# Kernel tuning notes

Measured on AMD Instinct MI355X. Metric: run time of the kernel, lower is better.

## Reference

```python
import jax, jax.numpy as jnp
import numpy as np

B, L, DM = 4, 1024, 1024
ED, N, K, R = 2048, 16, 4, 64  # d_inner, d_state, d_conv, dt_rank


def setup_inputs() -> dict:
    key = jax.random.key(0)
    ks = jax.random.split(key, 9)
    s = lambda i, shape, scale: jax.random.normal(ks[i], shape, jnp.float32) * scale
    inp = s(0, (B, L, DM), 1.0)
    W_in = s(1, (2 * ED, DM), DM ** -0.5)
    conv_w = s(2, (ED, 1, K), 0.5)
    conv_b = s(3, (ED,), 0.1)
    W_x = s(4, (R + 2 * N, ED), ED ** -0.5)
    W_dt = s(5, (ED, R), R ** -0.5)
    # dt bias init as in torch: inverse-softplus of dt ~ LogUniform(1e-3, 1e-1)
    dt = jnp.exp(jax.random.uniform(ks[6], (ED,)) * (np.log(0.1) - np.log(1e-3)) + np.log(1e-3))
    b_dt = dt + jnp.log(-jnp.expm1(-dt))
    A_log = jnp.log(jnp.tile(jnp.arange(1, N + 1, dtype=jnp.float32), (ED, 1)))
    D_param = jnp.ones((ED,), jnp.float32)
    W_out = s(7, (DM, ED), ED ** -0.5)
    return dict(input=inp, W_in=W_in, conv_w=conv_w, conv_b=conv_b, W_x=W_x,
                W_dt=W_dt, b_dt=b_dt, A_log=A_log, D_param=D_param, W_out=W_out)


def reference(input, W_in, conv_w, conv_b, W_x, W_dt, b_dt, A_log, D_param, W_out):
    b = input.shape[0]
    # in_proj -> x, z each [B, L, ED]
    xz = input @ W_in.T
    x, z = jnp.split(xz, 2, axis=-1)
    # causal depthwise conv over time (torch pads K-1 then crops to L == left-pad K-1)
    xc = jnp.transpose(x, (0, 2, 1))  # [B, ED, L]
    xc = jax.lax.conv_general_dilated(
        xc, conv_w, window_strides=(1,), padding=[(K - 1, 0)],
        dimension_numbers=('NCH', 'OIH', 'NCH'), feature_group_count=ED)
    xc = xc + conv_b[None, :, None]
    x = jax.nn.silu(jnp.transpose(xc, (0, 2, 1)))  # [B, L, ED]
    # x_proj -> delta_low, B, C
    dBC = x @ W_x.T  # [B, L, R+2N]
    dlow, Bm, Cm = dBC[..., :R], dBC[..., R:R + N], dBC[..., R + N:]
    # dt_proj (bias folded into softplus, matching delta_bias + delta_softplus)
    delta = jax.nn.softplus(dlow @ W_dt.T + b_dt)  # [B, L, ED]
    A = -jnp.exp(A_log)  # [ED, N]

    def step(h, ins):
        x_t, d_t, B_t, C_t = ins  # [B,ED],[B,ED],[B,N],[B,N]
        dA = jnp.exp(d_t[..., None] * A)           # [B, ED, N]
        h = dA * h + (d_t * x_t)[..., None] * B_t[:, None, :]
        y_t = jnp.einsum('ben,bn->be', h, C_t)
        return h, y_t

    h0 = jnp.zeros((b, ED, N), x.dtype)
    xs = (jnp.moveaxis(x, 1, 0), jnp.moveaxis(delta, 1, 0),
          jnp.moveaxis(Bm, 1, 0), jnp.moveaxis(Cm, 1, 0))
    _, ys = jax.lax.scan(step, h0, xs)
    y = jnp.moveaxis(ys, 0, 1) + D_param * x  # skip connection D*x
    y = y * jax.nn.silu(z)                    # output gating
    return y @ W_out.T                        # out_proj [B, L, DM]
```

## Files before the change

kernel.cpp:

```cpp
#include <hip/hip_runtime.h>
#include <hip/hip_bf16.h>
#include <math.h>

constexpr int Bb = 4, Ls = 1024, DMm = 1024, ED = 2048, Nst = 16, Rr = 64;
constexpr int Mrows = Bb * Ls;
constexpr int XZW = 2 * ED;
constexpr int NC = 32, CL = Ls / NC;

typedef __attribute__((ext_vector_type(8))) short bf16x8;
typedef __attribute__((ext_vector_type(4))) float f32x4;

#define GLOAD_LDS16(gp, lp) __builtin_amdgcn_global_load_lds( \
    (const __attribute__((address_space(1))) void*)(gp), \
    (__attribute__((address_space(3))) void*)(lp), 16, 0, 0)

#define SBAR() do { __builtin_amdgcn_sched_barrier(0); \
                    __builtin_amdgcn_s_barrier(); \
                    __builtin_amdgcn_sched_barrier(0); } while (0)
#define VMCNT4() do { asm volatile("s_waitcnt vmcnt(4)" ::: "memory"); \
                      __builtin_amdgcn_sched_barrier(0); } while (0)
#define VMCNT0() do { asm volatile("s_waitcnt vmcnt(0)" ::: "memory"); \
                      __builtin_amdgcn_sched_barrier(0); } while (0)

static __device__ __forceinline__ unsigned short f2bf(float x) {
    __hip_bfloat16 h = __float2bfloat16(x);
    return *reinterpret_cast<unsigned short*>(&h);
}
static __device__ __forceinline__ float bf2f(unsigned short u) {
    return __uint_as_float(((unsigned)u) << 16);
}

__global__ __launch_bounds__(256)
void cast5(const float* __restrict__ a, unsigned short* __restrict__ oa,
           const float* __restrict__ b, unsigned short* __restrict__ ob,
           const float* __restrict__ c, unsigned short* __restrict__ oc,
           const float* __restrict__ d, unsigned short* __restrict__ odh,
           unsigned short* __restrict__ odl,
           const float* __restrict__ e, unsigned short* __restrict__ oe)
{
    const int bid = blockIdx.x;
    if (bid < 10240) {
        const float* src; unsigned short* dst; int i;
        if (bid < 4096)      { src = a; dst = oa; i = (bid * 256 + threadIdx.x) * 4; }
        else if (bid < 8192) { src = b; dst = ob; i = ((bid - 4096) * 256 + threadIdx.x) * 4; }
        else                 { src = c; dst = oc; i = ((bid - 8192) * 256 + threadIdx.x) * 4; }
        float4 v = *(const float4*)(src + i);
        ushort4 o;
        o.x = f2bf(v.x); o.y = f2bf(v.y); o.z = f2bf(v.z); o.w = f2bf(v.w);
        *(ushort4*)(dst + i) = o;
    } else if (bid < 10368) {
        const int i = ((bid - 10240) * 256 + threadIdx.x) * 4;
        float4 v = *(const float4*)(d + i);
        ushort4 h, lo;
        h.x = f2bf(v.x); h.y = f2bf(v.y); h.z = f2bf(v.z); h.w = f2bf(v.w);
        lo.x = f2bf(v.x - bf2f(h.x)); lo.y = f2bf(v.y - bf2f(h.y));
        lo.z = f2bf(v.z - bf2f(h.z)); lo.w = f2bf(v.w - bf2f(h.w));
        *(ushort4*)(odh + i) = h;
        *(ushort4*)(odl + i) = lo;
    } else {
        const int i = ((bid - 10368) * 256 + threadIdx.x) * 4;
        float4 v = *(const float4*)(e + i);
        ushort4 o;
        o.x = f2bf(v.x); o.y = f2bf(v.y); o.z = f2bf(v.z); o.w = f2bf(v.w);
        *(ushort4*)(oe + i) = o;
    }
}

__global__ __launch_bounds__(512, 2)
void gemm256(const unsigned short* __restrict__ A,
             const unsigned short* __restrict__ B,
             unsigned short* __restrict__ C, int K, int ldc, int nbx)
{
    __shared__ unsigned short lds[65536];

    const int tid = threadIdx.x;
    const int l = tid & 63;
    const int w = tid >> 6;
    const int wm = w >> 2, wn = w & 3;

    const int cpx = gridDim.x >> 3;
    const int wg = (blockIdx.x & 7) * cpx + (blockIdx.x >> 3);
    const int bx = wg % nbx, by = wg / nbx;
    const int row0 = by * 256, col0 = bx * 256;

    const int NT = K >> 6;

    const int sr = l >> 3;
    const int sc = ((l & 7) ^ sr) * 8;
    const unsigned short* gA = A + (size_t)(row0 + sr) * K + sc;
    const unsigned short* gB = B + (size_t)(col0 + sr) * K + sc;

#define STAGE_A(t, h) do { const int b_ = (t) & 1;                              \
    GLOAD_LDS16(gA + (size_t)((h) * 128 + w * 16) * K + (t) * 64,              \
                &lds[b_ * 32768 + ((h) * 128 + w * 16) * 64 + l * 8]);          \
    GLOAD_LDS16(gA + (size_t)((h) * 128 + w * 16 + 8) * K + (t) * 64,          \
                &lds[b_ * 32768 + ((h) * 128 + w * 16 + 8) * 64 + l * 8]);      \
} while (0)
#define STAGE_B(t, h) do { const int b_ = (t) & 1;                              \
    GLOAD_LDS16(gB + (size_t)((h) * 128 + w * 16) * K + (t) * 64,              \
                &lds[b_ * 32768 + 16384 + ((h) * 128 + w * 16) * 64 + l * 8]);  \
    GLOAD_LDS16(gB + (size_t)((h) * 128 + w * 16 + 8) * K + (t) * 64,          \
                &lds[b_ * 32768 + 16384 + ((h) * 128 + w * 16 + 8) * 64 + l * 8]); \
} while (0)

    const int r15 = l & 15, kl = l >> 4, l7 = l & 7;

    f32x4 acc[8][4] = {};

    STAGE_A(0, 0); STAGE_B(0, 0); STAGE_A(0, 1); STAGE_B(0, 1);
    if (NT > 1) { STAGE_A(1, 0); STAGE_B(1, 0); VMCNT4(); }
    else        { VMCNT0(); }
    SBAR();

    for (int t = 0; t < NT; ++t) {
        const int base = (t & 1) * 32768;
        #pragma unroll
        for (int p = 0; p < 4; ++p) {
            const int mq = p >> 1, nq = p & 1;

            bf16x8 af[4][2], bfr[2][2];
            #pragma unroll
            for (int mf = 0; mf < 4; ++mf)
                #pragma unroll
                for (int ks = 0; ks < 2; ++ks) {
                    const int row = mq * 128 + wm * 64 + mf * 16 + r15;
                    const int slot = (ks * 4 + kl) ^ l7;
                    af[mf][ks] = *(const bf16x8*)&lds[base + row * 64 + slot * 8];
                }
            #pragma unroll
            for (int nf = 0; nf < 2; ++nf)
                #pragma unroll
                for (int ks = 0; ks < 2; ++ks) {
                    const int row = nq * 128 + wn * 32 + nf * 16 + r15;
                    const int slot = (ks * 4 + kl) ^ l7;
                    bfr[nf][ks] = *(const bf16x8*)&lds[base + 16384 + row * 64 + slot * 8];
                }

            if (p == 0 && t + 1 < NT) STAGE_A(t + 1, 1);
            if (p == 1 && t + 1 < NT) STAGE_B(t + 1, 1);
            if (p == 2 && t + 2 < NT) STAGE_A(t + 2, 0);
            if (p == 3 && t + 2 < NT) STAGE_B(t + 2, 0);

            __builtin_amdgcn_s_setprio(1);
            #pragma unroll
            for (int mf = 0; mf < 4; ++mf)
                #pragma unroll
                for (int nf = 0; nf < 2; ++nf)
                    #pragma unroll
                    for (int ks = 0; ks < 2; ++ks)
                        acc[mq * 4 + mf][nq * 2 + nf] =
                            __builtin_amdgcn_mfma_f32_16x16x32_bf16(
                                af[mf][ks], bfr[nf][ks],
                                acc[mq * 4 + mf][nq * 2 + nf], 0, 0, 0);
            __builtin_amdgcn_s_setprio(0);

            if (p < 3) {
                SBAR();
            } else {
                if (t + 2 < NT)      { VMCNT4(); SBAR(); }
                else if (t + 1 < NT) { VMCNT0(); SBAR(); }
            }
        }
    }

    const int crow = (l >> 4) * 4;
    #pragma unroll
    for (int am = 0; am < 8; ++am) {
        const int mq = am >> 2, mf = am & 3;
        #pragma unroll
        for (int bn = 0; bn < 4; ++bn) {
            const int nq = bn >> 1, nf = bn & 1;
            const int r = row0 + mq * 128 + wm * 64 + mf * 16 + crow;
            const int c = col0 + nq * 128 + wn * 32 + nf * 16 + r15;
            #pragma unroll
            for (int q = 0; q < 4; ++q)
                C[(size_t)(r + q) * ldc + c] = f2bf(acc[am][bn][q]);
        }
    }
#undef STAGE_A
#undef STAGE_B
}

__global__ __launch_bounds__(256)
void gemm_out(const unsigned short* __restrict__ A,
              const unsigned short* __restrict__ B,
              float* __restrict__ C, int K, int ldc)
{
    __shared__ unsigned short lds[2][(128 + 64) * 64];

    const int tid = threadIdx.x;
    const int l = tid & 63, w = tid >> 6;
    const int wm = w >> 1, wn = w & 1;
    const int row0 = blockIdx.y * 128, col0 = blockIdx.x * 64;

    const int sr = l >> 3;
    const int scS = ((l & 7) ^ sr) * 8;
    const unsigned short* gA = A + (size_t)(row0 + sr) * K + scS;
    const unsigned short* gB = B + (size_t)(col0 + sr) * K + scS;

#define STAGE6(t, bsel) do {                                                   \
    const size_t kt_ = (size_t)(t) * 64;                                       \
    _Pragma("unroll")                                                          \
    for (int i_ = 0; i_ < 4; ++i_) {                                           \
        const int rA_ = w * 32 + i_ * 8;                                       \
        GLOAD_LDS16(gA + (size_t)rA_ * K + kt_, &lds[(bsel)][rA_ * 64 + l * 8]); } \
    _Pragma("unroll")                                                          \
    for (int i_ = 0; i_ < 2; ++i_) {                                           \
        const int rB_ = w * 16 + i_ * 8;                                       \
        GLOAD_LDS16(gB + (size_t)rB_ * K + kt_, &lds[(bsel)][8192 + rB_ * 64 + l * 8]); } \
} while (0)

    const int r15 = l & 15, kl = l >> 4;
    const int NT = K >> 6;

    f32x4 acc[4][2] = {};

    STAGE6(0, 0);
    __syncthreads();

    int buf = 0;
    for (int t = 0; t < NT; ++t) {
        if (t + 1 < NT) STAGE6(t + 1, buf ^ 1);

        bf16x8 a[4][2], b[2][2];
        #pragma unroll
        for (int mf = 0; mf < 4; ++mf)
            #pragma unroll
            for (int ks = 0; ks < 2; ++ks) {
                const int row = wm * 64 + mf * 16 + r15;
                const int slot = (ks * 4 + kl) ^ (row & 7);
                a[mf][ks] = *(const bf16x8*)&lds[buf][row * 64 + slot * 8];
            }
        #pragma unroll
        for (int nf = 0; nf < 2; ++nf)
            #pragma unroll
            for (int ks = 0; ks < 2; ++ks) {
                const int row = wn * 32 + nf * 16 + r15;
                const int slot = (ks * 4 + kl) ^ (row & 7);
                b[nf][ks] = *(const bf16x8*)&lds[buf][8192 + row * 64 + slot * 8];
            }

        #pragma unroll
        for (int mf = 0; mf < 4; ++mf)
            #pragma unroll
            for (int nf = 0; nf < 2; ++nf)
                #pragma unroll
                for (int ks = 0; ks < 2; ++ks)
                    acc[mf][nf] = __builtin_amdgcn_mfma_f32_16x16x32_bf16(
                        a[mf][ks], b[nf][ks], acc[mf][nf], 0, 0, 0);

        __syncthreads();
        buf ^= 1;
    }

    const int crow = (l >> 4) * 4;
    #pragma unroll
    for (int mf = 0; mf < 4; ++mf)
        #pragma unroll
        for (int nf = 0; nf < 2; ++nf) {
            const int r = row0 + wm * 64 + mf * 16 + crow;
            const int c = col0 + wn * 32 + nf * 16 + r15;
            #pragma unroll
            for (int q = 0; q < 4; ++q)
                C[(size_t)(r + q) * ldc + c] = acc[mf][nf][q];
        }
#undef STAGE6
}

__global__ __launch_bounds__(256)
void gemm_bc(const unsigned short* __restrict__ A,
             const unsigned short* __restrict__ B,
             float* __restrict__ part)
{
    __shared__ unsigned short sA[2][128 * 64];
    __shared__ unsigned short sB[2][96 * 64];

    const int tid = threadIdx.x;
    const int l = tid & 63, w = tid >> 6;
    const int wm = w >> 1, wn = w & 1;
    const int row0 = blockIdx.y * 128;
    const int k0 = blockIdx.z * 256;

    const int lr = l >> 3;
    const int scS = ((l & 7) ^ lr) * 8;
    const int ldsOff = lr * 64 + (l & 7) * 8;

#define STAGE_BC(t, bsel) do {                                                  \
    const int kb_ = k0 + (t) * 64;                                              \
    _Pragma("unroll")                                                           \
    for (int p_ = 0; p_ < 4; ++p_) {                                            \
        const int r_ = p_ * 32 + w * 8;                                         \
        GLOAD_LDS16(A + (size_t)(row0 + r_ + lr) * 2048 + kb_ + scS,           \
                    &sA[(bsel)][r_ * 64 + ldsOff]); }                           \
    _Pragma("unroll")                                                           \
    for (int p_ = 0; p_ < 3; ++p_) {                                            \
        const int r_ = p_ * 32 + w * 8;                                         \
        GLOAD_LDS16(B + (size_t)(r_ + lr) * 2048 + kb_ + scS,                  \
                    &sB[(bsel)][r_ * 64 + ldsOff]); }                           \
} while (0)

    const int r15 = l & 15, kl = l >> 4;
    f32x4 acc[4][3] = {};

    STAGE_BC(0, 0);
    __syncthreads();

    int buf = 0;
    #pragma unroll
    for (int t = 0; t < 4; ++t) {
        if (t + 1 < 4) STAGE_BC(t + 1, buf ^ 1);

        bf16x8 a[4][2], b[3][2];
        #pragma unroll
        for (int mf = 0; mf < 4; ++mf)
            #pragma unroll
            for (int ks = 0; ks < 2; ++ks) {
                const int row = wm * 64 + mf * 16 + r15;
                const int slot = (ks * 4 + kl) ^ (row & 7);
                a[mf][ks] = *(const bf16x8*)&sA[buf][row * 64 + slot * 8];
            }
        #pragma unroll
        for (int nf = 0; nf < 3; ++nf)
            #pragma unroll
            for (int ks = 0; ks < 2; ++ks) {
                const int row = wn * 48 + nf * 16 + r15;
                const int slot = (ks * 4 + kl) ^ (row & 7);
                b[nf][ks] = *(const bf16x8*)&sB[buf][row * 64 + slot * 8];
            }

        #pragma unroll
        for (int mf = 0; mf < 4; ++mf)
            #pragma unroll
            for (int nf = 0; nf < 3; ++nf)
                #pragma unroll
                for (int ks = 0; ks < 2; ++ks)
                    acc[mf][nf] = __builtin_amdgcn_mfma_f32_16x16x32_bf16(
                        a[mf][ks], b[nf][ks], acc[mf][nf], 0, 0, 0);

        __syncthreads();
        buf ^= 1;
    }

    float* Cp = part + (size_t)blockIdx.z * (Mrows * 96);
    const int crow = (l >> 4) * 4;
    #pragma unroll
    for (int mf = 0; mf < 4; ++mf)
        #pragma unroll
        for (int nf = 0; nf < 3; ++nf) {
            const int r = row0 + wm * 64 + mf * 16 + crow;
            const int c = wn * 48 + nf * 16 + r15;
            #pragma unroll
            for (int q = 0; q < 4; ++q)
                Cp[(size_t)(r + q) * 96 + c] = acc[mf][nf][q];
        }
#undef STAGE_BC
}

__global__ __launch_bounds__(256)
void gemm_dt(const unsigned short* __restrict__ Ah,
             const unsigned short* __restrict__ Al,
             const unsigned short* __restrict__ Bh,
             const unsigned short* __restrict__ Bl,
             const float* __restrict__ bias,
             float* __restrict__ C)
{
    __shared__ unsigned short sAh[128 * 64], sAl[128 * 64];
    __shared__ unsigned short sBh[128 * 64], sBl[128 * 64];

    const int tid = threadIdx.x;
    const int l = tid & 63, w = tid >> 6;
    const int wm = w >> 1, wn = w & 1;
    const int row0 = blockIdx.y * 128, col0 = blockIdx.x * 128;

    const int lr = l >> 3;
    const int scS = ((l & 7) ^ lr) * 8;
    const int ldsOff = lr * 64 + (l & 7) * 8;

    #pragma unroll
    for (int p = 0; p < 4; ++p) {
        const int r = p * 32 + w * 8;
        GLOAD_LDS16(Ah + (size_t)(row0 + r + lr) * 64 + scS, &sAh[r * 64 + ldsOff]);
        GLOAD_LDS16(Al + (size_t)(row0 + r + lr) * 64 + scS, &sAl[r * 64 + ldsOff]);
        GLOAD_LDS16(Bh + (size_t)(col0 + r + lr) * 64 + scS, &sBh[r * 64 + ldsOff]);
        GLOAD_LDS16(Bl + (size_t)(col0 + r + lr) * 64 + scS, &sBl[r * 64 + ldsOff]);
    }
    __syncthreads();

    const int r15 = l & 15, kl = l >> 4;

    bf16x8 ah[4][2], al[4][2];
    #pragma unroll
    for (int mf = 0; mf < 4; ++mf)
        #pragma unroll
        for (int ks = 0; ks < 2; ++ks) {
            const int row = wm * 64 + mf * 16 + r15;
            const int slot = (ks * 4 + kl) ^ (row & 7);
            ah[mf][ks] = *(const bf16x8*)&sAh[row * 64 + slot * 8];
            al[mf][ks] = *(const bf16x8*)&sAl[row * 64 + slot * 8];
        }

    f32x4 acc[4][4] = {};
    #pragma unroll
    for (int nf = 0; nf < 4; ++nf) {
        bf16x8 bh[2], blo[2];
        #pragma unroll
        for (int ks = 0; ks < 2; ++ks) {
            const int row = wn * 64 + nf * 16 + r15;
            const int slot = (ks * 4 + kl) ^ (row & 7);
            bh[ks]  = *(const bf16x8*)&sBh[row * 64 + slot * 8];
            blo[ks] = *(const bf16x8*)&sBl[row * 64 + slot * 8];
        }
        #pragma unroll
        for (int mf = 0; mf < 4; ++mf)
            #pragma unroll
            for (int ks = 0; ks < 2; ++ks) {
                acc[mf][nf] = __builtin_amdgcn_mfma_f32_16x16x32_bf16(
                    ah[mf][ks], bh[ks], acc[mf][nf], 0, 0, 0);
                acc[mf][nf] = __builtin_amdgcn_mfma_f32_16x16x32_bf16(
                    ah[mf][ks], blo[ks], acc[mf][nf], 0, 0, 0);
                acc[mf][nf] = __builtin_amdgcn_mfma_f32_16x16x32_bf16(
                    al[mf][ks], bh[ks], acc[mf][nf], 0, 0, 0);
            }
    }

    const int crow = (l >> 4) * 4;
    #pragma unroll
    for (int mf = 0; mf < 4; ++mf)
        #pragma unroll
        for (int nf = 0; nf < 4; ++nf) {
            const int r = row0 + wm * 64 + mf * 16 + crow;
            const int c = col0 + wn * 64 + nf * 16 + r15;
            const float bb = bias[c];
            #pragma unroll
            for (int q = 0; q < 4; ++q) {
                float v = acc[mf][nf][q] + bb;
                v = (v > 20.f) ? v : log1pf(__expf(v));
                C[(size_t)(r + q) * 2048 + c] = v;
            }
        }
}

__global__ __launch_bounds__(256)
void reduce8(const float* __restrict__ part, float* __restrict__ outp,
             unsigned short* __restrict__ dlh, unsigned short* __restrict__ dll)
{
    constexpr size_t stride = (size_t)Mrows * 96;
    const size_t i = ((size_t)blockIdx.x * 256 + threadIdx.x) * 4;
    float4 s = *(const float4*)(part + i);
    #pragma unroll
    for (int k = 1; k < 8; ++k) {
        float4 v = *(const float4*)(part + k * stride + i);
        s.x += v.x; s.y += v.y; s.z += v.z; s.w += v.w;
    }
    *(float4*)(outp + i) = s;

    const int col = (int)(i % 96);
    if (col < 64) {
        const size_t row = i / 96;
        ushort4 h, lo;
        h.x = f2bf(s.x); h.y = f2bf(s.y); h.z = f2bf(s.z); h.w = f2bf(s.w);
        lo.x = f2bf(s.x - bf2f(h.x)); lo.y = f2bf(s.y - bf2f(h.y));
        lo.z = f2bf(s.z - bf2f(h.z)); lo.w = f2bf(s.w - bf2f(h.w));
        const size_t o = row * 64 + col;
        *(ushort4*)(dlh + o) = h;
        *(ushort4*)(dll + o) = lo;
    }
}

__global__ __launch_bounds__(256)
void conv_silu(const unsigned short* __restrict__ xz, const float* __restrict__ w,
               const float* __restrict__ cbias, unsigned short* __restrict__ out)
{
    const int idx = blockIdx.x * 256 + threadIdx.x;
    const int e = idx & (ED - 1);
    const int rq = idx >> 11;
    const int b = rq >> 8;
    const int l0 = (rq & 255) * 4;

    const unsigned short* base = xz + ((size_t)(b * Ls + l0)) * XZW + e;
    const float w0 = w[e * 4 + 0], w1 = w[e * 4 + 1],
                w2 = w[e * 4 + 2], w3 = w[e * 4 + 3];
    const float cb = cbias[e];

    float xm3 = 0.f, xm2 = 0.f, xm1 = 0.f;
    if (l0 > 0) {
        xm3 = bf2f(base[(ptrdiff_t)(-3) * XZW]);
        xm2 = bf2f(base[(ptrdiff_t)(-2) * XZW]);
        xm1 = bf2f(base[(ptrdiff_t)(-1) * XZW]);
    }
    const float x0 = bf2f(base[0]);
    const float x1 = bf2f(base[(size_t)1 * XZW]);
    const float x2 = bf2f(base[(size_t)2 * XZW]);
    const float x3 = bf2f(base[(size_t)3 * XZW]);

    float y[4];
    y[0] = cb + w0 * xm3 + w1 * xm2 + w2 * xm1 + w3 * x0;
    y[1] = cb + w0 * xm2 + w1 * xm1 + w2 * x0  + w3 * x1;
    y[2] = cb + w0 * xm1 + w1 * x0  + w2 * x1  + w3 * x2;
    y[3] = cb + w0 * x0  + w1 * x1  + w2 * x2  + w3 * x3;

    unsigned short* op = out + ((size_t)(b * Ls + l0)) * ED + e;
    #pragma unroll
    for (int j = 0; j < 4; ++j)
        op[(size_t)j * ED] = f2bf(y[j] / (1.f + __expf(-y[j])));
}

__global__ __launch_bounds__(256)
void scan_phaseA(const unsigned short* __restrict__ xconv,
                 const float* __restrict__ delta,
                 const float* __restrict__ dBC,
                 const float* __restrict__ A_log,
                 float* __restrict__ hA,
                 float* __restrict__ PA)
{
    __shared__ float sB[CL][16];
    const int t = threadIdx.x;
    const int e = blockIdx.x * 256 + t;
    const int ck = blockIdx.y;
    const int b = blockIdx.z;
    const int row0 = b * Ls + ck * CL;

    if (t < CL * 4) {
        const int r = t >> 2, c4 = (t & 3) * 4;
        *(float4*)&sB[r][c4] =
            *(const float4*)&dBC[(size_t)(row0 + r) * 96 + Rr + c4];
    }
    __syncthreads();

    float Ae[16];
    #pragma unroll
    for (int n = 0; n < 16; ++n) Ae[n] = -__expf(A_log[e * 16 + n]);

    float h[16] = {};
    float S = 0.f;
    const float* dp = delta + (size_t)row0 * ED + e;
    const unsigned short* xp = xconv + (size_t)row0 * ED + e;

    #pragma unroll 4
    for (int l = 0; l < CL; ++l) {
        const float d  = dp[(size_t)l * ED];
        const float xv = bf2f(xp[(size_t)l * ED]);
        const float dx = d * xv;
        S += d;
        const float4* bl = (const float4*)&sB[l][0];
        float Bv[16];
        #pragma unroll
        for (int q = 0; q < 4; ++q) {
            float4 t4 = bl[q];
            Bv[4*q] = t4.x; Bv[4*q+1] = t4.y; Bv[4*q+2] = t4.z; Bv[4*q+3] = t4.w;
        }
        #pragma unroll
        for (int n = 0; n < 16; ++n) {
            const float dA = __expf(d * Ae[n]);
            h[n] = fmaf(dA, h[n], dx * Bv[n]);
        }
    }

    float* hp = hA + ((size_t)(b * NC + ck) * 16) * ED + e;
    float* pp = PA + ((size_t)(b * NC + ck) * 16) * ED + e;
    #pragma unroll
    for (int n = 0; n < 16; ++n) {
        hp[(size_t)n * ED] = h[n];
        pp[(size_t)n * ED] = __expf(S * Ae[n]);
    }
}

__global__ __launch_bounds__(256)
void scan_phaseB(float* __restrict__ hA, const float* __restrict__ PA)
{
    const int id = blockIdx.x * 256 + threadIdx.x;
    const int e = id & (ED - 1);
    const int n = (id >> 11) & 15;
    const int b = id >> 15;
    float h = 0.f;
    #pragma unroll
    for (int c = 0; c < NC; ++c) {
        const size_t o = ((size_t)((b * NC + c) * 16 + n)) * ED + e;
        const float loc = hA[o];
        hA[o] = h;
        h = fmaf(PA[o], h, loc);
    }
}

__global__ __launch_bounds__(256)
void scan_phaseC(const unsigned short* __restrict__ xconv,
                 const float* __restrict__ delta,
                 const float* __restrict__ dBC,
                 const unsigned short* __restrict__ xz,
                 const float* __restrict__ A_log,
                 const float* __restrict__ Dp,
                 const float* __restrict__ hA,
                 unsigned short* __restrict__ ybf)
{
    __shared__ float sBC[CL][32];
    const int t = threadIdx.x;
    const int e = blockIdx.x * 256 + t;
    const int ck = blockIdx.y;
    const int b = blockIdx.z;
    const int row0 = b * Ls + ck * CL;

    {
        const int r = t >> 3, c4 = (t & 7) * 4;
        *(float4*)&sBC[r][c4] =
            *(const float4*)&dBC[(size_t)(row0 + r) * 96 + Rr + c4];
    }
    __syncthreads();

    float Ae[16];
    #pragma unroll
    for (int n = 0; n < 16; ++n) Ae[n] = -__expf(A_log[e * 16 + n]);
    const float De = Dp[e];

    float h[16];
    const float* hp = hA + ((size_t)(b * NC + ck) * 16) * ED + e;
    #pragma unroll
    for (int n = 0; n < 16; ++n) h[n] = hp[(size_t)n * ED];

    const float* dp = delta + (size_t)row0 * ED + e;
    const unsigned short* xp = xconv + (size_t)row0 * ED + e;
    const unsigned short* zp = xz + (size_t)row0 * XZW + ED + e;
    unsigned short* yp = ybf + (size_t)row0 * ED + e;

    #pragma unroll 2
    for (int l = 0; l < CL; ++l) {
        const float d  = dp[(size_t)l * ED];
        const float xv = bf2f(xp[(size_t)l * ED]);
        const float dx = d * xv;
        const float4* bl = (const float4*)&sBC[l][0];
        float Bv[16], Cv[16];
        #pragma unroll
        for (int q = 0; q < 4; ++q) {
            float4 t4 = bl[q];
            Bv[4*q] = t4.x; Bv[4*q+1] = t4.y; Bv[4*q+2] = t4.z; Bv[4*q+3] = t4.w;
            float4 u4 = bl[4 + q];
            Cv[4*q] = u4.x; Cv[4*q+1] = u4.y; Cv[4*q+2] = u4.z; Cv[4*q+3] = u4.w;
        }
        float yv = 0.f;
        #pragma unroll
        for (int n = 0; n < 16; ++n) {
            const float dA = __expf(d * Ae[n]);
            h[n] = fmaf(dA, h[n], dx * Bv[n]);
            yv = fmaf(h[n], Cv[n], yv);
        }
        const float zv = bf2f(zp[(size_t)l * XZW]);
        const float sz = zv / (1.f + __expf(-zv));
        yp[(size_t)l * ED] = f2bf((yv + De * xv) * sz);
    }
}

extern "C" void kernel_launch(void* const* d_in, const int* in_sizes, int n_in,
                              void* d_out, int out_size, void* d_ws, size_t ws_size,
                              hipStream_t stream)
{
    const float* input  = (const float*)d_in[0];
    const float* W_in   = (const float*)d_in[1];
    const float* conv_w = (const float*)d_in[2];
    const float* conv_b = (const float*)d_in[3];
    const float* W_x    = (const float*)d_in[4];
    const float* W_dt   = (const float*)d_in[5];
    const float* b_dt   = (const float*)d_in[6];
    const float* A_log  = (const float*)d_in[7];
    const float* Dp     = (const float*)d_in[8];
    const float* W_out  = (const float*)d_in[9];
    float* out = (float*)d_out;
    float* ws  = (float*)d_ws;

    float* xzR   = ws;
    float* xconv = xzR   + (size_t)16777216;
    float* dBC   = xconv + (size_t)8388608;
    float* delta = dBC   + (size_t)393216;
    float* hA    = delta + (size_t)8388608;
    float* PA    = hA    + (size_t)4194304;
    float* wob   = PA    + (size_t)4194304;
    float* extra = wob   + (size_t)1048576;

    unsigned short* xz_bf   = (unsigned short*)xzR;
    unsigned short* xconv_bf= (unsigned short*)xconv;
    unsigned short* in_bf   = (unsigned short*)(xconv + 4194304);
    unsigned short* Win_bf  = (unsigned short*)(xconv + 6291456);
    unsigned short* Wout_bf = (unsigned short*)wob;
    float*          parts   = hA;
    unsigned short* y_bf    = (unsigned short*)PA;

    unsigned short* dlow_hi = (unsigned short*)extra;
    unsigned short* dlow_lo = dlow_hi + 262144;
    unsigned short* Wdt_hi  = dlow_lo + 262144;
    unsigned short* Wdt_lo  = Wdt_hi + 131072;
    unsigned short* Wx_bf   = Wdt_lo + 131072;

    const dim3 blk(256);

    cast5<<<10560, blk, 0, stream>>>(input, in_bf, W_in, Win_bf, W_out, Wout_bf,
                                     W_dt, Wdt_hi, Wdt_lo, W_x, Wx_bf);

    gemm256<<<(XZW / 256) * (Mrows / 256), dim3(512), 0, stream>>>(
        in_bf, Win_bf, xz_bf, DMm, XZW, XZW / 256);

    conv_silu<<<(Mrows / 4) * ED / 256, blk, 0, stream>>>(
        xz_bf, conv_w, conv_b, xconv_bf);

    gemm_bc<<<dim3(1, Mrows / 128, 8), blk, 0, stream>>>(xconv_bf, Wx_bf, parts);
    reduce8<<<(Mrows * 96) / 1024, blk, 0, stream>>>(parts, dBC, dlow_hi, dlow_lo);

    gemm_dt<<<dim3(ED / 128, Mrows / 128), blk, 0, stream>>>(
        dlow_hi, dlow_lo, Wdt_hi, Wdt_lo, b_dt, delta);

    scan_phaseA<<<dim3(ED / 256, NC, Bb), blk, 0, stream>>>(
        xconv_bf, delta, dBC, A_log, hA, PA);
    scan_phaseB<<<(Bb * 16 * ED) / 256, blk, 0, stream>>>(hA, PA);
    scan_phaseC<<<dim3(ED / 256, NC, Bb), blk, 0, stream>>>(
        xconv_bf, delta, dBC, xz_bf, A_log, Dp, hA, y_bf);

    gemm_out<<<dim3(DMm / 64, Mrows / 128), blk, 0, stream>>>(
        y_bf, Wout_bf, out, ED, DMm);
}
```

Measured before the change: 210.5 us.

## Store delta and chunk scan states in bf16, reuse fragments in gemm256

The delta tensor from gemm_dt and the per-chunk scan state and decay products (hA, PA) are now written and read as bf16 instead of fp32. This halves the memory traffic of the three scan phases, which are bandwidth-bound. The main GEMM loop is also restructured to reuse the loaded A and B fragments across quadrants, which cuts redundant LDS reads. The trade-off is lower precision in delta and in the carried scan states, which may increase numerical error in the recurrence.

```diff
diff --git a/kernel.cpp b/kernel.cpp
--- a/kernel.cpp
+++ b/kernel.cpp
@@ -103,6 +103,33 @@
                 &lds[b_ * 32768 + 16384 + ((h) * 128 + w * 16 + 8) * 64 + l * 8]); \
 } while (0)
 
+#define LOAD_AF(dst, mq_) do { _Pragma("unroll")                                \
+    for (int mf_ = 0; mf_ < 4; ++mf_) { _Pragma("unroll")                       \
+    for (int ks_ = 0; ks_ < 2; ++ks_) {                                         \
+        const int row_ = (mq_) * 128 + wm * 64 + mf_ * 16 + r15;                \
+        const int slot_ = (ks_ * 4 + kl) ^ l7;                                  \
+        dst[mf_][ks_] = *(const bf16x8*)&lds[base + row_ * 64 + slot_ * 8]; } } \
+} while (0)
+#define LOAD_BF(dst, nq_) do { _Pragma("unroll")                                \
+    for (int nf_ = 0; nf_ < 2; ++nf_) { _Pragma("unroll")                       \
+    for (int ks_ = 0; ks_ < 2; ++ks_) {                                         \
+        const int row_ = (nq_) * 128 + wn * 32 + nf_ * 16 + r15;                \
+        const int slot_ = (ks_ * 4 + kl) ^ l7;                                  \
+        dst[nf_][ks_] = *(const bf16x8*)&lds[base + 16384 + row_ * 64 + slot_ * 8]; } } \
+} while (0)
+#define MFMA16(afv, bfv, mq_, nq_) do {                                         \
+    __builtin_amdgcn_s_setprio(1);                                              \
+    _Pragma("unroll")                                                           \
+    for (int mf_ = 0; mf_ < 4; ++mf_) { _Pragma("unroll")                       \
+    for (int nf_ = 0; nf_ < 2; ++nf_) { _Pragma("unroll")                       \
+    for (int ks_ = 0; ks_ < 2; ++ks_)                                           \
+        acc[(mq_) * 4 + mf_][(nq_) * 2 + nf_] =                                 \
+            __builtin_amdgcn_mfma_f32_16x16x32_bf16(                            \
+                afv[mf_][ks_], bfv[nf_][ks_],                                   \
+                acc[(mq_) * 4 + mf_][(nq_) * 2 + nf_], 0, 0, 0); } }            \
+    __builtin_amdgcn_s_setprio(0);                                              \
+} while (0)
+
     const int r15 = l & 15, kl = l >> 4, l7 = l & 7;
 
     f32x4 acc[8][4] = {};
@@ -114,53 +141,27 @@
 
     for (int t = 0; t < NT; ++t) {
         const int base = (t & 1) * 32768;
-        #pragma unroll
-        for (int p = 0; p < 4; ++p) {
-            const int mq = p >> 1, nq = p & 1;
-
-            bf16x8 af[4][2], bfr[2][2];
-            #pragma unroll
-            for (int mf = 0; mf < 4; ++mf)
-                #pragma unroll
-                for (int ks = 0; ks < 2; ++ks) {
-                    const int row = mq * 128 + wm * 64 + mf * 16 + r15;
-                    const int slot = (ks * 4 + kl) ^ l7;
-                    af[mf][ks] = *(const bf16x8*)&lds[base + row * 64 + slot * 8];
-                }
-            #pragma unroll
-            for (int nf = 0; nf < 2; ++nf)
-                #pragma unroll
-                for (int ks = 0; ks < 2; ++ks) {
-                    const int row = nq * 128 + wn * 32 + nf * 16 + r15;
-                    const int slot = (ks * 4 + kl) ^ l7;
-                    bfr[nf][ks] = *(const bf16x8*)&lds[base + 16384 + row * 64 + slot * 8];
-                }
-
-            if (p == 0 && t + 1 < NT) STAGE_A(t + 1, 1);
-            if (p == 1 && t + 1 < NT) STAGE_B(t + 1, 1);
-            if (p == 2 && t + 2 < NT) STAGE_A(t + 2, 0);
-            if (p == 3 && t + 2 < NT) STAGE_B(t + 2, 0);
-
-            __builtin_amdgcn_s_setprio(1);
-            #pragma unroll
-            for (int mf = 0; mf < 4; ++mf)
-                #pragma unroll
-                for (int nf = 0; nf < 2; ++nf)
-                    #pragma unroll
-                    for (int ks = 0; ks < 2; ++ks)
-                        acc[mq * 4 + mf][nq * 2 + nf] =
-                            __builtin_amdgcn_mfma_f32_16x16x32_bf16(
-                                af[mf][ks], bfr[nf][ks],
-                                acc[mq * 4 + mf][nq * 2 + nf], 0, 0, 0);
-            __builtin_amdgcn_s_setprio(0);
-
-            if (p < 3) {
-                SBAR();
-            } else {
-                if (t + 2 < NT)      { VMCNT4(); SBAR(); }
-                else if (t + 1 < NT) { VMCNT0(); SBAR(); }
-            }
-        }
+        bf16x8 af[4][2], bf0[2][2], bf1[2][2];
+
+        LOAD_AF(af, 0); LOAD_BF(bf0, 0);
+        if (t + 1 < NT) STAGE_A(t + 1, 1);
+        MFMA16(af, bf0, 0, 0);
+        SBAR();
+
+        LOAD_BF(bf1, 1);
+        if (t + 1 < NT) STAGE_B(t + 1, 1);
+        MFMA16(af, bf1, 0, 1);
+        SBAR();
+
+        LOAD_AF(af, 1);
+        if (t + 2 < NT) STAGE_A(t + 2, 0);
+        MFMA16(af, bf0, 1, 0);
+        SBAR();
+
+        if (t + 2 < NT) STAGE_B(t + 2, 0);
+        MFMA16(af, bf1, 1, 1);
+        if (t + 2 < NT)      { VMCNT4(); SBAR(); }
+        else if (t + 1 < NT) { VMCNT0(); SBAR(); }
     }
 
     const int crow = (l >> 4) * 4;
@@ -179,6 +180,9 @@
     }
 #undef STAGE_A
 #undef STAGE_B
+#undef LOAD_AF
+#undef LOAD_BF
+#undef MFMA16
 }
 
 __global__ __launch_bounds__(256)
@@ -362,7 +366,7 @@
              const unsigned short* __restrict__ Bh,
              const unsigned short* __restrict__ Bl,
              const float* __restrict__ bias,
-             float* __restrict__ C)
+             unsigned short* __restrict__ C)
 {
     __shared__ unsigned short sAh[128 * 64], sAl[128 * 64];
     __shared__ unsigned short sBh[128 * 64], sBl[128 * 64];
@@ -435,7 +439,7 @@
             for (int q = 0; q < 4; ++q) {
                 float v = acc[mf][nf][q] + bb;
                 v = (v > 20.f) ? v : log1pf(__expf(v));
-                C[(size_t)(r + q) * 2048 + c] = v;
+                C[(size_t)(r + q) * 2048 + c] = f2bf(v);
             }
         }
 }
@@ -507,11 +511,11 @@
 
 __global__ __launch_bounds__(256)
 void scan_phaseA(const unsigned short* __restrict__ xconv,
-                 const float* __restrict__ delta,
+                 const unsigned short* __restrict__ delta,
                  const float* __restrict__ dBC,
                  const float* __restrict__ A_log,
-                 float* __restrict__ hA,
-                 float* __restrict__ PA)
+                 unsigned short* __restrict__ hA,
+                 unsigned short* __restrict__ PA)
 {
     __shared__ float sB[CL][16];
     const int t = threadIdx.x;
@@ -533,12 +537,12 @@
 
     float h[16] = {};
     float S = 0.f;
-    const float* dp = delta + (size_t)row0 * ED + e;
+    const unsigned short* dp = delta + (size_t)row0 * ED + e;
     const unsigned short* xp = xconv + (size_t)row0 * ED + e;
 
     #pragma unroll 4
     for (int l = 0; l < CL; ++l) {
-        const float d  = dp[(size_t)l * ED];
+        const float d  = bf2f(dp[(size_t)l * ED]);
         const float xv = bf2f(xp[(size_t)l * ED]);
         const float dx = d * xv;
         S += d;
@@ -556,17 +560,17 @@
         }
     }
 
-    float* hp = hA + ((size_t)(b * NC + ck) * 16) * ED + e;
-    float* pp = PA + ((size_t)(b * NC + ck) * 16) * ED + e;
+    unsigned short* hp = hA + ((size_t)(b * NC + ck) * 16) * ED + e;
+    unsigned short* pp = PA + ((size_t)(b * NC + ck) * 16) * ED + e;
     #pragma unroll
     for (int n = 0; n < 16; ++n) {
-        hp[(size_t)n * ED] = h[n];
-        pp[(size_t)n * ED] = __expf(S * Ae[n]);
-    }
-}
-
-__global__ __launch_bounds__(256)
-void scan_phaseB(float* __restrict__ hA, const float* __restrict__ PA)
+        hp[(size_t)n * ED] = f2bf(h[n]);
+        pp[(size_t)n * ED] = f2bf(__expf(S * Ae[n]));
+    }
+}
+
+__global__ __launch_bounds__(256)
+void scan_phaseB(unsigned short* __restrict__ hA, const unsigned short* __restrict__ PA)
 {
     const int id = blockIdx.x * 256 + threadIdx.x;
     const int e = id & (ED - 1);
@@ -576,20 +580,20 @@
     #pragma unroll
     for (int c = 0; c < NC; ++c) {
         const size_t o = ((size_t)((b * NC + c) * 16 + n)) * ED + e;
-        const float loc = hA[o];
-        hA[o] = h;
-        h = fmaf(PA[o], h, loc);
+        const float loc = bf2f(hA[o]);
+        hA[o] = f2bf(h);
+        h = fmaf(bf2f(PA[o]), h, loc);
     }
 }
 
 __global__ __launch_bounds__(256)
 void scan_phaseC(const unsigned short* __restrict__ xconv,
-                 const float* __restrict__ delta,
+                 const unsigned short* __restrict__ delta,
                  const float* __restrict__ dBC,
                  const unsigned short* __restrict__ xz,
                  const float* __restrict__ A_log,
                  const float* __restrict__ Dp,
-                 const float* __restrict__ hA,
+                 const unsigned short* __restrict__ hA,
                  unsigned short* __restrict__ ybf)
 {
     __shared__ float sBC[CL][32];
@@ -612,18 +616,18 @@
     const float De = Dp[e];
 
     float h[16];
-    const float* hp = hA + ((size_t)(b * NC + ck) * 16) * ED + e;
-    #pragma unroll
-    for (int n = 0; n < 16; ++n) h[n] = hp[(size_t)n * ED];
-
-    const float* dp = delta + (size_t)row0 * ED + e;
+    const unsigned short* hp = hA + ((size_t)(b * NC + ck) * 16) * ED + e;
+    #pragma unroll
+    for (int n = 0; n < 16; ++n) h[n] = bf2f(hp[(size_t)n * ED]);
+
+    const unsigned short* dp = delta + (size_t)row0 * ED + e;
     const unsigned short* xp = xconv + (size_t)row0 * ED + e;
     const unsigned short* zp = xz + (size_t)row0 * XZW + ED + e;
     unsigned short* yp = ybf + (size_t)row0 * ED + e;
 
     #pragma unroll 2
     for (int l = 0; l < CL; ++l) {
-        const float d  = dp[(size_t)l * ED];
+        const float d  = bf2f(dp[(size_t)l * ED]);
         const float xv = bf2f(xp[(size_t)l * ED]);
         const float dx = d * xv;
         const float4* bl = (const float4*)&sBC[l][0];
@@ -674,13 +678,16 @@
     float* wob   = PA    + (size_t)4194304;
     float* extra = wob   + (size_t)1048576;
 
-    unsigned short* xz_bf   = (unsigned short*)xzR;
-    unsigned short* xconv_bf= (unsigned short*)xconv;
-    unsigned short* in_bf   = (unsigned short*)(xconv + 4194304);
-    unsigned short* Win_bf  = (unsigned short*)(xconv + 6291456);
-    unsigned short* Wout_bf = (unsigned short*)wob;
-    float*          parts   = hA;
-    unsigned short* y_bf    = (unsigned short*)PA;
+    unsigned short* xz_bf    = (unsigned short*)xzR;
+    unsigned short* xconv_bf = (unsigned short*)xconv;
+    unsigned short* in_bf    = (unsigned short*)(xconv + 4194304);
+    unsigned short* Win_bf   = (unsigned short*)(xconv + 6291456);
+    unsigned short* y_bf     = (unsigned short*)(xconv + 4194304);
+    unsigned short* Wout_bf  = (unsigned short*)wob;
+    unsigned short* delta_bf = (unsigned short*)delta;
+    unsigned short* hA_bf    = (unsigned short*)hA;
+    unsigned short* PA_bf    = (unsigned short*)PA;
+    float*          parts    = hA;
 
     unsigned short* dlow_hi = (unsigned short*)extra;
     unsigned short* dlow_lo = dlow_hi + 262144;
@@ -703,13 +710,13 @@
     reduce8<<<(Mrows * 96) / 1024, blk, 0, stream>>>(parts, dBC, dlow_hi, dlow_lo);
 
     gemm_dt<<<dim3(ED / 128, Mrows / 128), blk, 0, stream>>>(
-        dlow_hi, dlow_lo, Wdt_hi, Wdt_lo, b_dt, delta);
+        dlow_hi, dlow_lo, Wdt_hi, Wdt_lo, b_dt, delta_bf);
 
     scan_phaseA<<<dim3(ED / 256, NC, Bb), blk, 0, stream>>>(
-        xconv_bf, delta, dBC, A_log, hA, PA);
-    scan_phaseB<<<(Bb * 16 * ED) / 256, blk, 0, stream>>>(hA, PA);
+        xconv_bf, delta_bf, dBC, A_log, hA_bf, PA_bf);
+    scan_phaseB<<<(Bb * 16 * ED) / 256, blk, 0, stream>>>(hA_bf, PA_bf);
     scan_phaseC<<<dim3(ED / 256, NC, Bb), blk, 0, stream>>>(
-        xconv_bf, delta, dBC, xz_bf, A_log, Dp, hA, y_bf);
+        xconv_bf, delta_bf, dBC, xz_bf, A_log, Dp, hA_bf, y_bf);
 
     gemm_out<<<dim3(DMm / 64, Mrows / 128), blk, 0, stream>>>(
         y_bf, Wout_bf, out, ED, DMm);
```

Result: faster. 205.4 us (-2.4%).
